# Performance work log

Hardware: AMD Instinct MI355X
Metric: run time of the kernel (lower is better)

The kernel has to match this reference:

```python
import jax, jax.numpy as jnp
import numpy as np

DIM = 256
N_EMBED = 8192


def setup_inputs() -> dict:
    key = jax.random.key(0)
    k1, k2 = jax.random.split(key)
    x = jax.random.normal(k1, (16, 32, 32, DIM), dtype=jnp.float32)
    embed = jax.random.normal(k2, (DIM, N_EMBED), dtype=jnp.float32)
    return {"x": x, "embed": embed}


def reference(x, embed):
    # x: [B, H, W, D]; embed: [D, K]
    D = embed.shape[0]
    flat = x.reshape(-1, D)  # [N, D]
    dist = (
        jnp.sum(flat * flat, axis=1, keepdims=True)
        - 2.0 * (flat @ embed)
        + jnp.sum(embed * embed, axis=0, keepdims=True)
    )  # [N, K]
    embed_ind = jnp.argmin(dist, axis=1)  # argmax of -dist
    embed_ind = embed_ind.reshape(x.shape[:-1])  # [B, H, W]
    quantize = jnp.take(embed.T, embed_ind, axis=0)  # [B, H, W, D]
    diff = jnp.mean((jax.lax.stop_gradient(quantize) - x) ** 2)
    quantize = x + jax.lax.stop_gradient(quantize - x)  # straight-through
    return quantize, diff, embed_ind
```

## Files before the change

### kernel.cpp

```cpp
#include <hip/hip_runtime.h>

typedef unsigned long long u64;
typedef unsigned short ushort_t;
typedef float f32x4 __attribute__((ext_vector_type(4)));
typedef short bf16x8 __attribute__((ext_vector_type(8)));
typedef unsigned short ushort8 __attribute__((ext_vector_type(8)));

#define D_DIM   256
#define N_ROWS  16384
#define K_CODES 8192
#define OFF_DIFF 4194304
#define OFF_IND  4194305

#define XH_OFF    0ULL
#define XL_OFF    8388608ULL
#define EHT_OFF   16777216ULL
#define ELT_OFF   20971520ULL
#define ETF_OFF   25165824ULL
#define ENORM_OFF 33554432ULL
#define KEYS_OFF  33587200ULL
#define PV1_OFF   33718272ULL
#define PIDX_OFF  37912576ULL
#define PV2_OFF   42106880ULL
#define WLC_OFF   46301184ULL
#define WL_OFF    46301440ULL
#define PART_OFF  46366976ULL
#define WS_NEED   46375168ULL

#define MARGIN_TH 0.08f

#define GLD(gp, lp) __builtin_amdgcn_global_load_lds( \
    (const __attribute__((address_space(1))) unsigned int*)(const void*)(gp), \
    (__attribute__((address_space(3))) unsigned int*)(void*)(lp), 16, 0, 0)

__device__ __forceinline__ unsigned int fsort(float f) {
    unsigned int u = __float_as_uint(f);
    return (u & 0x80000000u) ? ~u : (u | 0x80000000u);
}
__device__ __forceinline__ ushort_t f2bf(float f) {
    unsigned int u = __float_as_uint(f);
    unsigned int r = (u + 0x7fffu + ((u >> 16) & 1u)) >> 16;
    return (ushort_t)r;
}
__device__ __forceinline__ float bf2f(ushort_t h) {
    return __uint_as_float(((unsigned int)h) << 16);
}

__global__ __launch_bounds__(256) void k_split_x(const float* __restrict__ x,
                                                 ushort_t* __restrict__ xh,
                                                 ushort_t* __restrict__ xl) {
    int base = (blockIdx.x * 256 + threadIdx.x) * 8;
    float4 v0 = *reinterpret_cast<const float4*>(&x[base]);
    float4 v1 = *reinterpret_cast<const float4*>(&x[base + 4]);
    float f[8] = {v0.x, v0.y, v0.z, v0.w, v1.x, v1.y, v1.z, v1.w};
    ushort8 h, l;
    #pragma unroll
    for (int i = 0; i < 8; ++i) {
        ushort_t hb = f2bf(f[i]);
        h[i] = (short)hb;
        l[i] = (short)f2bf(f[i] - bf2f(hb));
    }
    *reinterpret_cast<ushort8*>(&xh[base]) = h;
    *reinterpret_cast<ushort8*>(&xl[base]) = l;
}

__global__ __launch_bounds__(256) void k_split_eT(const float* __restrict__ e,
                                                  ushort_t* __restrict__ ehT,
                                                  ushort_t* __restrict__ elT,
                                                  float* __restrict__ eTf) {
    __shared__ float tile[64][257];
    const int t = threadIdx.x;
    const int c0 = blockIdx.x * 64;
    for (int it = 0; it < 64; ++it) {
        int d = it * 4 + (t >> 6);
        tile[t & 63][d] = e[d * K_CODES + c0 + (t & 63)];
    }
    __syncthreads();
    for (int cc = 0; cc < 64; ++cc) {
        float v = tile[cc][t];
        ushort_t hb = f2bf(v);
        size_t o = (size_t)(c0 + cc) * 256 + t;
        ehT[o] = hb;
        elT[o] = f2bf(v - bf2f(hb));
        eTf[o] = v;
    }
}

__global__ __launch_bounds__(256) void k_norms(const float* __restrict__ e,
                                               float* __restrict__ enorm,
                                               int* __restrict__ wlc) {
    int k = blockIdx.x * 256 + threadIdx.x;
    float s = 0.f;
    #pragma unroll 8
    for (int d = 0; d < D_DIM; ++d) {
        float v = e[d * K_CODES + k];
        s = fmaf(v, v, s);
    }
    enorm[k] = s;
    if (k == 0) *wlc = 0;
}

__global__ __launch_bounds__(256, 3) void k_mfma(const ushort_t* __restrict__ xh,
                                                 const ushort_t* __restrict__ xl,
                                                 const ushort_t* __restrict__ ehT,
                                                 const ushort_t* __restrict__ elT,
                                                 const float* __restrict__ enorm,
                                                 float* __restrict__ pv1,
                                                 int* __restrict__ pidx,
                                                 float* __restrict__ pv2) {
    __shared__ short Ah[4096], Al[4096], Bh[4096], Bl[4096];
    __shared__ float mg_v1[2][128];
    __shared__ float mg_v2[2][128];
    __shared__ int   mg_i1[2][128];
    const int tid = threadIdx.x;
    const int l = tid & 63, w = tid >> 6;
    const int wm = w >> 1, wn = w & 1;
    const int r0 = blockIdx.x * 128;
    const int c0 = blockIdx.y * 128;

    const int rl = l >> 2;
    const int g = (l & 3) ^ ((rl >> 1) & 3);
    const int rowL0 = w * 32 + rl;
    const size_t aoff = (size_t)(c0 + rowL0) * 256 + g * 8;
    const size_t boff = (size_t)(r0 + rowL0) * 256 + g * 8;
    short* Adst  = Ah + w * 1024;
    short* Aldst = Al + w * 1024;
    short* Bdst  = Bh + w * 1024;
    short* Bldst = Bl + w * 1024;

    const int fr = l & 15, kg = l >> 4;

    f32x4 acc[4][4];
    #pragma unroll
    for (int mi = 0; mi < 4; ++mi)
        #pragma unroll
        for (int ni = 0; ni < 4; ++ni)
            #pragma unroll
            for (int q = 0; q < 4; ++q) acc[mi][ni][q] = 0.f;

    for (int kt = 0; kt < 8; ++kt) {
        const int ko = kt * 32;
        GLD(&ehT[aoff + ko], Adst);
        GLD(&ehT[aoff + ko + 4096], Adst + 512);
        GLD(&elT[aoff + ko], Aldst);
        GLD(&elT[aoff + ko + 4096], Aldst + 512);
        GLD(&xh[boff + ko], Bdst);
        GLD(&xh[boff + ko + 4096], Bdst + 512);
        GLD(&xl[boff + ko], Bldst);
        GLD(&xl[boff + ko + 4096], Bldst + 512);
        __syncthreads();

        bf16x8 a_h[4], a_l[4], b_h[4], b_l[4];
        #pragma unroll
        for (int mi = 0; mi < 4; ++mi) {
            int rf = wn * 64 + mi * 16 + fr;
            int idx = rf * 32 + ((kg ^ ((rf >> 1) & 3)) * 8);
            a_h[mi] = *reinterpret_cast<const bf16x8*>(&Ah[idx]);
            a_l[mi] = *reinterpret_cast<const bf16x8*>(&Al[idx]);
        }
        #pragma unroll
        for (int ni = 0; ni < 4; ++ni) {
            int cf = wm * 64 + ni * 16 + fr;
            int idx = cf * 32 + ((kg ^ ((cf >> 1) & 3)) * 8);
            b_h[ni] = *reinterpret_cast<const bf16x8*>(&Bh[idx]);
            b_l[ni] = *reinterpret_cast<const bf16x8*>(&Bl[idx]);
        }
        #pragma unroll
        for (int mi = 0; mi < 4; ++mi)
            #pragma unroll
            for (int ni = 0; ni < 4; ++ni) {
                acc[mi][ni] = __builtin_amdgcn_mfma_f32_16x16x32_bf16(a_h[mi], b_h[ni], acc[mi][ni], 0, 0, 0);
                acc[mi][ni] = __builtin_amdgcn_mfma_f32_16x16x32_bf16(a_h[mi], b_l[ni], acc[mi][ni], 0, 0, 0);
                acc[mi][ni] = __builtin_amdgcn_mfma_f32_16x16x32_bf16(a_l[mi], b_h[ni], acc[mi][ni], 0, 0, 0);
            }
        __syncthreads();
    }

    float v1[4], v2[4];
    int   i1[4];
    #pragma unroll
    for (int ni = 0; ni < 4; ++ni) { v1[ni] = 1e30f; v2[ni] = 1e30f; i1[ni] = 0; }

    float en_r[4][4];
    #pragma unroll
    for (int mi = 0; mi < 4; ++mi)
        #pragma unroll
        for (int r = 0; r < 4; ++r)
            en_r[mi][r] = enorm[c0 + wn * 64 + mi * 16 + kg * 4 + r];
    const int cwn = c0 + wn * 64 + kg * 4;

    #pragma unroll
    for (int ni = 0; ni < 4; ++ni)
        #pragma unroll
        for (int mi = 0; mi < 4; ++mi)
            #pragma unroll
            for (int r = 0; r < 4; ++r) {
                float dv = fmaf(-2.f, acc[mi][ni][r], en_r[mi][r]);
                int c = cwn + mi * 16 + r;
                if (dv < v1[ni]) { v2[ni] = v1[ni]; v1[ni] = dv; i1[ni] = c; }
                else v2[ni] = fminf(v2[ni], dv);
            }

    #pragma unroll
    for (int ni = 0; ni < 4; ++ni) {
        #pragma unroll
        for (int m = 16; m <= 32; m <<= 1) {
            float ov1 = __shfl_xor(v1[ni], m, 64);
            int   oi1 = __shfl_xor(i1[ni], m, 64);
            float ov2 = __shfl_xor(v2[ni], m, 64);
            bool better = (ov1 < v1[ni]) || (ov1 == v1[ni] && oi1 < i1[ni]);
            float nv2 = fminf(fminf(v2[ni], ov2), better ? v1[ni] : ov1);
            if (better) { v1[ni] = ov1; i1[ni] = oi1; }
            v2[ni] = nv2;
        }
        if (l < 16) {
            int lr = wm * 64 + ni * 16 + l;
            mg_v1[wn][lr] = v1[ni];
            mg_i1[wn][lr] = i1[ni];
            mg_v2[wn][lr] = v2[ni];
        }
    }

    __syncthreads();
    if (tid < 128) {
        float v1a = mg_v1[0][tid], v2a = mg_v2[0][tid];
        float v1b = mg_v1[1][tid], v2b = mg_v2[1][tid];
        int   i1a = mg_i1[0][tid], i1b = mg_i1[1][tid];
        bool better = (v1b < v1a) || (v1b == v1a && i1b < i1a);
        float fv1 = better ? v1b : v1a;
        int   fi1 = better ? i1b : i1a;
        float fv2 = fminf(fminf(v2a, v2b), better ? v1a : v1b);
        int pos = (r0 + tid) * 64 + blockIdx.y;
        pv1[pos] = fv1; pidx[pos] = fi1; pv2[pos] = fv2;
    }
}

__global__ __launch_bounds__(256) void k_reduce(const float* __restrict__ pv1,
                                                const int* __restrict__ pidx,
                                                const float* __restrict__ pv2,
                                                u64* __restrict__ keys,
                                                int* __restrict__ wlc,
                                                int* __restrict__ wl) {
    const int w = threadIdx.x >> 6, l = threadIdx.x & 63;
    const int row = blockIdx.x * 4 + w;
    float v1 = pv1[row * 64 + l];
    int   i1 = pidx[row * 64 + l];
    float v2 = pv2[row * 64 + l];
    #pragma unroll
    for (int m = 1; m <= 32; m <<= 1) {
        float ov1 = __shfl_xor(v1, m, 64);
        int   oi1 = __shfl_xor(i1, m, 64);
        float ov2 = __shfl_xor(v2, m, 64);
        bool better = (ov1 < v1) || (ov1 == v1 && oi1 < i1);
        float nv2 = fminf(fminf(v2, ov2), better ? v1 : ov1);
        if (better) { v1 = ov1; i1 = oi1; }
        v2 = nv2;
    }
    if (l == 0) {
        if (v2 - v1 < MARGIN_TH) {
            int p = atomicAdd(wlc, 1);
            wl[p] = row;
            keys[row] = ~0ULL;
        } else {
            keys[row] = (((u64)fsort(v1)) << 32) | (unsigned int)i1;
        }
    }
}

__global__ __launch_bounds__(128) void k_exact(const float* __restrict__ x,
                                               const float* __restrict__ e,
                                               const float* __restrict__ enorm,
                                               const int* __restrict__ wlc,
                                               const int* __restrict__ wl,
                                               u64* __restrict__ keys) {
    __shared__ float xs[8][256];
    __shared__ int rowids[8];
    __shared__ u64 red[8][2];
    const int t = threadIdx.x;
    const int cnt = *wlc;
    const int c = blockIdx.x * 128 + t;
    const float en = enorm[c];

    for (int j = blockIdx.y; j * 8 < cnt; j += 16) {
        int nr = cnt - j * 8; if (nr > 8) nr = 8;
        if (t < 8) rowids[t] = (t < nr) ? wl[j * 8 + t] : 0;
        __syncthreads();
        for (int rr = 0; rr < nr; ++rr) {
            int row = rowids[rr];
            xs[rr][t] = x[(size_t)row * 256 + t];
            xs[rr][t + 128] = x[(size_t)row * 256 + t + 128];
        }
        __syncthreads();
        float dot[8];
        #pragma unroll
        for (int rr = 0; rr < 8; ++rr) dot[rr] = 0.f;
        for (int d = 0; d < 256; ++d) {
            float ev = e[d * K_CODES + c];
            #pragma unroll
            for (int rr = 0; rr < 8; ++rr) dot[rr] = fmaf(ev, xs[rr][d], dot[rr]);
        }
        #pragma unroll
        for (int rr = 0; rr < 8; ++rr) {
            float dist = fmaf(-2.f, dot[rr], en);
            u64 kk = (((u64)fsort(dist)) << 32) | (unsigned int)c;
            #pragma unroll
            for (int m = 1; m <= 32; m <<= 1) {
                u64 ok = __shfl_xor(kk, m, 64);
                kk = ok < kk ? ok : kk;
            }
            if ((t & 63) == 0) red[rr][t >> 6] = kk;
        }
        __syncthreads();
        if (t < nr) {
            u64 fk = red[t][0] < red[t][1] ? red[t][0] : red[t][1];
            atomicMin(&keys[rowids[t]], fk);
        }
        __syncthreads();
    }
}

__global__ __launch_bounds__(256) void k_gather2(const float* __restrict__ x,
                                                 const float* __restrict__ eTf,
                                                 const u64* __restrict__ keys,
                                                 float* __restrict__ out_q,
                                                 float* __restrict__ out_ind,
                                                 float* __restrict__ partial) {
    const int t = threadIdx.x, w = t >> 6, l = t & 63;
    float s = 0.f;
    #pragma unroll
    for (int p = 0; p < 2; ++p) {
        int row = blockIdx.x * 8 + p * 4 + w;
        int idx = (int)(keys[row] & 0xFFFFFFFFu);
        float4 q = *reinterpret_cast<const float4*>(&eTf[(size_t)idx * 256 + l * 4]);
        float4 xv = *reinterpret_cast<const float4*>(&x[(size_t)row * 256 + l * 4]);
        *reinterpret_cast<float4*>(&out_q[(size_t)row * 256 + l * 4]) = q;
        if (l == 0) out_ind[row] = (float)idx;
        float dx = q.x - xv.x, dy = q.y - xv.y, dz = q.z - xv.z, dw = q.w - xv.w;
        s += dx * dx + dy * dy + dz * dz + dw * dw;
    }
    #pragma unroll
    for (int m = 1; m <= 32; m <<= 1) s += __shfl_xor(s, m, 64);
    __shared__ float red[4];
    if (l == 0) red[w] = s;
    __syncthreads();
    if (t == 0) partial[blockIdx.x] = red[0] + red[1] + red[2] + red[3];
}

__global__ __launch_bounds__(256) void k_diff(const float* __restrict__ partial,
                                              float* __restrict__ out_diff) {
    const int t = threadIdx.x;
    float s = 0.f;
    for (int i = t; i < 2048; i += 256) s += partial[i];
    #pragma unroll
    for (int m = 1; m <= 32; m <<= 1) s += __shfl_xor(s, m, 64);
    __shared__ float red[4];
    if ((t & 63) == 0) red[t >> 6] = s;
    __syncthreads();
    if (t == 0) out_diff[0] = (red[0] + red[1] + red[2] + red[3]) * (1.0f / 4194304.0f);
}

constexpr int FBM = 64, FBN = 256, FBK = 32, FNSPLIT = 2;

__global__ __launch_bounds__(256) void k_init_fb(u64* __restrict__ keys,
                                                 float* __restrict__ diff_slot) {
    int t = blockIdx.x * 256 + threadIdx.x;
    if (t < N_ROWS) keys[t] = ~0ULL;
    if (t == 0) diff_slot[0] = 0.0f;
}

__global__ __launch_bounds__(256) void k_argmin_fb(const float* __restrict__ x,
                                                   const float* __restrict__ e,
                                                   const float* __restrict__ enorm,
                                                   u64* __restrict__ keys) {
    __shared__ float xs[FBK][FBM + 4];
    __shared__ float es[FBK][FBN];
    const int tid = threadIdx.x;
    const int tr = tid >> 5, tc = tid & 31;
    const int row0 = blockIdx.x * FBM;
    const int cbase = blockIdx.y * (K_CODES / FNSPLIT);
    float minv[8]; int mini[8];
    #pragma unroll
    for (int i = 0; i < 8; ++i) { minv[i] = 1e30f; mini[i] = 0; }
    for (int chunk = 0; chunk < (K_CODES / FNSPLIT) / FBN; ++chunk) {
        const int c0 = cbase + chunk * FBN;
        float acc[8][8];
        #pragma unroll
        for (int i = 0; i < 8; ++i)
            #pragma unroll
            for (int j = 0; j < 8; ++j) acc[i][j] = 0.f;
        for (int kt = 0; kt < D_DIM / FBK; ++kt) {
            #pragma unroll
            for (int l2 = 0; l2 < 2; ++l2) {
                int q = tid + 256 * l2, r = q >> 3, kq = q & 7;
                float4 v = *reinterpret_cast<const float4*>(&x[(row0 + r) * D_DIM + kt * FBK + kq * 4]);
                xs[kq * 4 + 0][r] = v.x; xs[kq * 4 + 1][r] = v.y;
                xs[kq * 4 + 2][r] = v.z; xs[kq * 4 + 3][r] = v.w;
            }
            #pragma unroll
            for (int l2 = 0; l2 < 8; ++l2) {
                int q = tid + 256 * l2, k = q >> 6, cq = q & 63;
                float4 v = *reinterpret_cast<const float4*>(&e[(kt * FBK + k) * K_CODES + c0 + cq * 4]);
                *reinterpret_cast<float4*>(&es[k][cq * 4]) = v;
            }
            __syncthreads();
            #pragma unroll 8
            for (int k = 0; k < FBK; ++k) {
                float4 a0 = *reinterpret_cast<const float4*>(&xs[k][tr * 8]);
                float4 a1 = *reinterpret_cast<const float4*>(&xs[k][tr * 8 + 4]);
                float4 b0 = *reinterpret_cast<const float4*>(&es[k][tc * 8]);
                float4 b1 = *reinterpret_cast<const float4*>(&es[k][tc * 8 + 4]);
                float a[8] = {a0.x, a0.y, a0.z, a0.w, a1.x, a1.y, a1.z, a1.w};
                float b[8] = {b0.x, b0.y, b0.z, b0.w, b1.x, b1.y, b1.z, b1.w};
                #pragma unroll
                for (int i = 0; i < 8; ++i)
                    #pragma unroll
                    for (int j = 0; j < 8; ++j) acc[i][j] = fmaf(a[i], b[j], acc[i][j]);
            }
            __syncthreads();
        }
        #pragma unroll
        for (int j = 0; j < 8; ++j) {
            int c = c0 + tc * 8 + j;
            float en = enorm[c];
            #pragma unroll
            for (int i = 0; i < 8; ++i) {
                float dv = fmaf(-2.0f, acc[i][j], en);
                if (dv < minv[i]) { minv[i] = dv; mini[i] = c; }
            }
        }
    }
    #pragma unroll
    for (int m = 16; m >= 1; m >>= 1) {
        #pragma unroll
        for (int i = 0; i < 8; ++i) {
            float ov = __shfl_xor(minv[i], m, 64);
            int oi = __shfl_xor(mini[i], m, 64);
            if (ov < minv[i] || (ov == minv[i] && oi < mini[i])) { minv[i] = ov; mini[i] = oi; }
        }
    }
    if (tc == 0) {
        #pragma unroll
        for (int i = 0; i < 8; ++i) {
            int row = row0 + tr * 8 + i;
            u64 key = (((u64)fsort(minv[i])) << 32) | (unsigned int)mini[i];
            atomicMin(&keys[row], key);
        }
    }
}

__global__ __launch_bounds__(256) void k_gather_fb(const float* __restrict__ x,
                                                   const float* __restrict__ e,
                                                   const u64* __restrict__ keys,
                                                   float* __restrict__ out_q,
                                                   float* __restrict__ out_diff,
                                                   float* __restrict__ out_ind) {
    int row = blockIdx.x, d = threadIdx.x;
    int idx = (int)(keys[row] & 0xFFFFFFFFu);
    float q = e[d * K_CODES + idx];
    float xv = x[row * D_DIM + d];
    out_q[row * D_DIM + d] = q;
    if (d == 0) out_ind[row] = (float)idx;
    float sq = q - xv; sq *= sq;
    #pragma unroll
    for (int m = 32; m >= 1; m >>= 1) sq += __shfl_xor(sq, m, 64);
    __shared__ float red[4];
    if ((d & 63) == 0) red[d >> 6] = sq;
    __syncthreads();
    if (d == 0) {
        float s = (red[0] + red[1] + red[2] + red[3]) * (1.0f / (float)(N_ROWS * D_DIM));
        atomicAdd(out_diff, s);
    }
}

extern "C" void kernel_launch(void* const* d_in, const int* in_sizes, int n_in,
                              void* d_out, int out_size, void* d_ws, size_t ws_size,
                              hipStream_t stream) {
    const float* x = (const float*)d_in[0];
    const float* e = (const float*)d_in[1];
    float* out = (float*)d_out;
    float* out_q = out;
    float* out_diff = out + OFF_DIFF;
    float* out_ind = out + OFF_IND;
    char* ws = (char*)d_ws;

    if (ws_size >= WS_NEED) {
        ushort_t* xh  = (ushort_t*)(ws + XH_OFF);
        ushort_t* xl  = (ushort_t*)(ws + XL_OFF);
        ushort_t* ehT = (ushort_t*)(ws + EHT_OFF);
        ushort_t* elT = (ushort_t*)(ws + ELT_OFF);
        float* eTf    = (float*)(ws + ETF_OFF);
        float* enorm  = (float*)(ws + ENORM_OFF);
        u64* keys     = (u64*)(ws + KEYS_OFF);
        float* pv1    = (float*)(ws + PV1_OFF);
        int* pidx     = (int*)(ws + PIDX_OFF);
        float* pv2    = (float*)(ws + PV2_OFF);
        int* wlc      = (int*)(ws + WLC_OFF);
        int* wl       = (int*)(ws + WL_OFF);
        float* part   = (float*)(ws + PART_OFF);

        k_split_x <<<2048, 256, 0, stream>>>(x, xh, xl);
        k_split_eT<<<128, 256, 0, stream>>>(e, ehT, elT, eTf);
        k_norms   <<<32, 256, 0, stream>>>(e, enorm, wlc);
        k_mfma    <<<dim3(128, 64), 256, 0, stream>>>(xh, xl, ehT, elT, enorm, pv1, pidx, pv2);
        k_reduce  <<<4096, 256, 0, stream>>>(pv1, pidx, pv2, keys, wlc, wl);
        k_exact   <<<dim3(64, 16), 128, 0, stream>>>(x, e, enorm, wlc, wl, keys);
        k_gather2 <<<2048, 256, 0, stream>>>(x, eTf, keys, out_q, out_ind, part);
        k_diff    <<<1, 256, 0, stream>>>(part, out_diff);
    } else {
        float* enorm = (float*)ws;
        u64* keys = (u64*)(ws + 32768);
        k_init_fb  <<<64, 256, 0, stream>>>(keys, out_diff);
        k_norms    <<<32, 256, 0, stream>>>(e, enorm, (int*)(ws + 163840));
        k_argmin_fb<<<dim3(N_ROWS / FBM, FNSPLIT), 256, 0, stream>>>(x, e, enorm, keys);
        k_gather_fb<<<N_ROWS, 256, 0, stream>>>(x, e, keys, out_q, out_diff, out_ind);
    }
}
```

Measured before the change: 338.7 us.

## Fuse prep kernels, drop fp32 transposed codebook, atomic diff reduction

Merges the x split, codebook transpose/split and norm kernels into one launch, using block-index ranges to pick the role. Vectorizes the transposed bf16 stores. Drops the fp32 transposed codebook copy: the gather rebuilds values as hi+lo bf16, which is only exact when the split loses nothing. Replaces the separate diff-reduction kernel with atomicAdd into the output, trading fewer launches and less write traffic for a nondeterministic summation order.

```diff
diff --git a/kernel.cpp b/kernel.cpp
--- a/kernel.cpp
+++ b/kernel.cpp
@@ -46,58 +46,66 @@
     return __uint_as_float(((unsigned int)h) << 16);
 }
 
-__global__ __launch_bounds__(256) void k_split_x(const float* __restrict__ x,
-                                                 ushort_t* __restrict__ xh,
-                                                 ushort_t* __restrict__ xl) {
-    int base = (blockIdx.x * 256 + threadIdx.x) * 8;
-    float4 v0 = *reinterpret_cast<const float4*>(&x[base]);
-    float4 v1 = *reinterpret_cast<const float4*>(&x[base + 4]);
-    float f[8] = {v0.x, v0.y, v0.z, v0.w, v1.x, v1.y, v1.z, v1.w};
-    ushort8 h, l;
-    #pragma unroll
-    for (int i = 0; i < 8; ++i) {
-        ushort_t hb = f2bf(f[i]);
-        h[i] = (short)hb;
-        l[i] = (short)f2bf(f[i] - bf2f(hb));
-    }
-    *reinterpret_cast<ushort8*>(&xh[base]) = h;
-    *reinterpret_cast<ushort8*>(&xl[base]) = l;
-}
-
-__global__ __launch_bounds__(256) void k_split_eT(const float* __restrict__ e,
-                                                  ushort_t* __restrict__ ehT,
-                                                  ushort_t* __restrict__ elT,
-                                                  float* __restrict__ eTf) {
+__global__ __launch_bounds__(256) void k_prep(const float* __restrict__ x,
+                                              const float* __restrict__ e,
+                                              ushort_t* __restrict__ xh,
+                                              ushort_t* __restrict__ xl,
+                                              ushort_t* __restrict__ ehT,
+                                              ushort_t* __restrict__ elT,
+                                              float* __restrict__ enorm,
+                                              int* __restrict__ wlc,
+                                              float* __restrict__ out_diff) {
     __shared__ float tile[64][257];
+    const int bid = blockIdx.x;
     const int t = threadIdx.x;
-    const int c0 = blockIdx.x * 64;
-    for (int it = 0; it < 64; ++it) {
-        int d = it * 4 + (t >> 6);
-        tile[t & 63][d] = e[d * K_CODES + c0 + (t & 63)];
-    }
-    __syncthreads();
-    for (int cc = 0; cc < 64; ++cc) {
-        float v = tile[cc][t];
-        ushort_t hb = f2bf(v);
-        size_t o = (size_t)(c0 + cc) * 256 + t;
-        ehT[o] = hb;
-        elT[o] = f2bf(v - bf2f(hb));
-        eTf[o] = v;
-    }
-}
-
-__global__ __launch_bounds__(256) void k_norms(const float* __restrict__ e,
-                                               float* __restrict__ enorm,
-                                               int* __restrict__ wlc) {
-    int k = blockIdx.x * 256 + threadIdx.x;
-    float s = 0.f;
-    #pragma unroll 8
-    for (int d = 0; d < D_DIM; ++d) {
-        float v = e[d * K_CODES + k];
-        s = fmaf(v, v, s);
-    }
-    enorm[k] = s;
-    if (k == 0) *wlc = 0;
+    if (bid < 2048) {
+        int base = (bid * 256 + t) * 8;
+        float4 v0 = *reinterpret_cast<const float4*>(&x[base]);
+        float4 v1 = *reinterpret_cast<const float4*>(&x[base + 4]);
+        float f[8] = {v0.x, v0.y, v0.z, v0.w, v1.x, v1.y, v1.z, v1.w};
+        ushort8 h, l;
+        #pragma unroll
+        for (int i = 0; i < 8; ++i) {
+            ushort_t hb = f2bf(f[i]);
+            h[i] = hb;
+            l[i] = f2bf(f[i] - bf2f(hb));
+        }
+        *reinterpret_cast<ushort8*>(&xh[base]) = h;
+        *reinterpret_cast<ushort8*>(&xl[base]) = l;
+    } else if (bid < 2176) {
+        const int c0 = (bid - 2048) * 64;
+        for (int it = 0; it < 64; ++it) {
+            int d = it * 4 + (t >> 6);
+            tile[t & 63][d] = e[d * K_CODES + c0 + (t & 63)];
+        }
+        __syncthreads();
+        #pragma unroll
+        for (int it = 0; it < 8; ++it) {
+            int cc = it * 8 + (t >> 5);
+            int d0 = (t & 31) * 8;
+            ushort8 h8, l8;
+            #pragma unroll
+            for (int j = 0; j < 8; ++j) {
+                float v = tile[cc][d0 + j];
+                ushort_t hb = f2bf(v);
+                h8[j] = hb;
+                l8[j] = f2bf(v - bf2f(hb));
+            }
+            size_t o = (size_t)(c0 + cc) * 256 + d0;
+            *reinterpret_cast<ushort8*>(&ehT[o]) = h8;
+            *reinterpret_cast<ushort8*>(&elT[o]) = l8;
+        }
+    } else {
+        int k = (bid - 2176) * 256 + t;
+        float s = 0.f;
+        #pragma unroll 8
+        for (int d = 0; d < D_DIM; ++d) {
+            float v = e[d * K_CODES + k];
+            s = fmaf(v, v, s);
+        }
+        enorm[k] = s;
+        if (k == 0) { *wlc = 0; out_diff[0] = 0.0f; }
+    }
 }
 
 __global__ __launch_bounds__(256, 3) void k_mfma(const ushort_t* __restrict__ xh,
@@ -320,43 +328,58 @@
 }
 
 __global__ __launch_bounds__(256) void k_gather2(const float* __restrict__ x,
-                                                 const float* __restrict__ eTf,
+                                                 const ushort_t* __restrict__ ehT,
+                                                 const ushort_t* __restrict__ elT,
                                                  const u64* __restrict__ keys,
                                                  float* __restrict__ out_q,
                                                  float* __restrict__ out_ind,
-                                                 float* __restrict__ partial) {
+                                                 float* __restrict__ out_diff) {
     const int t = threadIdx.x, w = t >> 6, l = t & 63;
+    const int row = blockIdx.x * 8 + w * 2 + (l >> 5);
+    const int d0 = (l & 31) * 8;
+    const int idx = (int)(keys[row] & 0xFFFFFFFFu);
+
+    ushort8 h8 = *reinterpret_cast<const ushort8*>(&ehT[(size_t)idx * 256 + d0]);
+    ushort8 l8 = *reinterpret_cast<const ushort8*>(&elT[(size_t)idx * 256 + d0]);
+    float4 xv0 = *reinterpret_cast<const float4*>(&x[(size_t)row * 256 + d0]);
+    float4 xv1 = *reinterpret_cast<const float4*>(&x[(size_t)row * 256 + d0 + 4]);
+    float xv[8] = {xv0.x, xv0.y, xv0.z, xv0.w, xv1.x, xv1.y, xv1.z, xv1.w};
+
+    float q[8];
     float s = 0.f;
     #pragma unroll
-    for (int p = 0; p < 2; ++p) {
-        int row = blockIdx.x * 8 + p * 4 + w;
-        int idx = (int)(keys[row] & 0xFFFFFFFFu);
-        float4 q = *reinterpret_cast<const float4*>(&eTf[(size_t)idx * 256 + l * 4]);
-        float4 xv = *reinterpret_cast<const float4*>(&x[(size_t)row * 256 + l * 4]);
-        *reinterpret_cast<float4*>(&out_q[(size_t)row * 256 + l * 4]) = q;
-        if (l == 0) out_ind[row] = (float)idx;
-        float dx = q.x - xv.x, dy = q.y - xv.y, dz = q.z - xv.z, dw = q.w - xv.w;
-        s += dx * dx + dy * dy + dz * dz + dw * dw;
-    }
+    for (int j = 0; j < 8; ++j) {
+        q[j] = bf2f(h8[j]) + bf2f(l8[j]);
+        float dq = q[j] - xv[j];
+        s = fmaf(dq, dq, s);
+    }
+    float4 q0 = {q[0], q[1], q[2], q[3]};
+    float4 q1 = {q[4], q[5], q[6], q[7]};
+    *reinterpret_cast<float4*>(&out_q[(size_t)row * 256 + d0]) = q0;
+    *reinterpret_cast<float4*>(&out_q[(size_t)row * 256 + d0 + 4]) = q1;
+    if (d0 == 0) out_ind[row] = (float)idx;
+
     #pragma unroll
     for (int m = 1; m <= 32; m <<= 1) s += __shfl_xor(s, m, 64);
     __shared__ float red[4];
     if (l == 0) red[w] = s;
     __syncthreads();
-    if (t == 0) partial[blockIdx.x] = red[0] + red[1] + red[2] + red[3];
-}
-
-__global__ __launch_bounds__(256) void k_diff(const float* __restrict__ partial,
-                                              float* __restrict__ out_diff) {
-    const int t = threadIdx.x;
+    if (t == 0)
+        atomicAdd(out_diff, (red[0] + red[1] + red[2] + red[3]) * (1.0f / 4194304.0f));
+}
+
+__global__ __launch_bounds__(256) void k_norms(const float* __restrict__ e,
+                                               float* __restrict__ enorm,
+                                               int* __restrict__ wlc) {
+    int k = blockIdx.x * 256 + threadIdx.x;
     float s = 0.f;
-    for (int i = t; i < 2048; i += 256) s += partial[i];
-    #pragma unroll
-    for (int m = 1; m <= 32; m <<= 1) s += __shfl_xor(s, m, 64);
-    __shared__ float red[4];
-    if ((t & 63) == 0) red[t >> 6] = s;
-    __syncthreads();
-    if (t == 0) out_diff[0] = (red[0] + red[1] + red[2] + red[3]) * (1.0f / 4194304.0f);
+    #pragma unroll 8
+    for (int d = 0; d < D_DIM; ++d) {
+        float v = e[d * K_CODES + k];
+        s = fmaf(v, v, s);
+    }
+    enorm[k] = s;
+    if (k == 0) *wlc = 0;
 }
 
 constexpr int FBM = 64, FBN = 256, FBK = 32, FNSPLIT = 2;
@@ -488,7 +511,6 @@
         ushort_t* xl  = (ushort_t*)(ws + XL_OFF);
         ushort_t* ehT = (ushort_t*)(ws + EHT_OFF);
         ushort_t* elT = (ushort_t*)(ws + ELT_OFF);
-        float* eTf    = (float*)(ws + ETF_OFF);
         float* enorm  = (float*)(ws + ENORM_OFF);
         u64* keys     = (u64*)(ws + KEYS_OFF);
         float* pv1    = (float*)(ws + PV1_OFF);
@@ -496,16 +518,12 @@
         float* pv2    = (float*)(ws + PV2_OFF);
         int* wlc      = (int*)(ws + WLC_OFF);
         int* wl       = (int*)(ws + WL_OFF);
-        float* part   = (float*)(ws + PART_OFF);
-
-        k_split_x <<<2048, 256, 0, stream>>>(x, xh, xl);
-        k_split_eT<<<128, 256, 0, stream>>>(e, ehT, elT, eTf);
-        k_norms   <<<32, 256, 0, stream>>>(e, enorm, wlc);
-        k_mfma    <<<dim3(128, 64), 256, 0, stream>>>(xh, xl, ehT, elT, enorm, pv1, pidx, pv2);
-        k_reduce  <<<4096, 256, 0, stream>>>(pv1, pidx, pv2, keys, wlc, wl);
-        k_exact   <<<dim3(64, 16), 128, 0, stream>>>(x, e, enorm, wlc, wl, keys);
-        k_gather2 <<<2048, 256, 0, stream>>>(x, eTf, keys, out_q, out_ind, part);
-        k_diff    <<<1, 256, 0, stream>>>(part, out_diff);
+
+        k_prep   <<<2208, 256, 0, stream>>>(x, e, xh, xl, ehT, elT, enorm, wlc, out_diff);
+        k_mfma   <<<dim3(128, 64), 256, 0, stream>>>(xh, xl, ehT, elT, enorm, pv1, pidx, pv2);
+        k_reduce <<<4096, 256, 0, stream>>>(pv1, pidx, pv2, keys, wlc, wl);
+        k_exact  <<<dim3(64, 16), 128, 0, stream>>>(x, e, enorm, wlc, wl, keys);
+        k_gather2<<<2048, 256, 0, stream>>>(x, ehT, elT, keys, out_q, out_ind, out_diff);
     } else {
         float* enorm = (float*)ws;
         u64* keys = (u64*)(ws + 32768);
```

New measurement: 351.0 us. 1.04x slower.
